# Kernel tuning notes

Hardware: AMD Instinct MI355X
Metric: run time of the kernel (lower is better)

## Reference

```python
import jax, jax.numpy as jnp
import numpy as np

N, D = 16384, 256

def setup_inputs() -> dict:
    key = jax.random.key(0)
    k1, k2, k3 = jax.random.split(key, 3)
    X = jax.random.normal(k1, (N, D), dtype=jnp.float32)
    W = jax.random.normal(k2, (D, D), dtype=jnp.float32) * (1.0 / np.sqrt(D))
    b = jax.random.normal(k3, (D,), dtype=jnp.float32) * (1.0 / np.sqrt(D))
    return {"X": X, "W": W, "b": b}

def reference(X, W, b):
    # Step 1: bilinear attention A = X W X^T   (N, N) -- materialized as in original
    A = (X @ W) @ X.T
    # Step 2: context aggregation Z = A X      (N, D)
    Z = A @ X
    # Step 3: output head g = Z b              (N,)
    g = Z @ b
    return g
```

## Files before the change

kernel.cpp:

```cpp
#include <hip/hip_runtime.h>

#define NROWS 16384
#define DDIM  256
#define K1BLK 2048
#define NSLOT 64


__global__ __launch_bounds__(256) void k1_v(const float* __restrict__ X,
                                            const float* __restrict__ b,
                                            float* __restrict__ slots) {
    const int tid  = threadIdx.x;
    const int lane = tid & 63;
    const int wave = tid >> 6;
    const int bid  = blockIdx.x;

    const float4* X4 = (const float4*)X;
    const float4  bf = ((const float4*)b)[lane];

    float4 vacc = make_float4(0.f, 0.f, 0.f, 0.f);
    const int row0 = bid * 8 + wave * 2;
    #pragma unroll
    for (int i = 0; i < 2; ++i) {
        const float4 xv = X4[(row0 + i) * 64 + lane];
        float t = xv.x * bf.x + xv.y * bf.y + xv.z * bf.z + xv.w * bf.w;
        #pragma unroll
        for (int off = 32; off; off >>= 1) t += __shfl_xor(t, off, 64);
        vacc.x += t * xv.x; vacc.y += t * xv.y;
        vacc.z += t * xv.z; vacc.w += t * xv.w;
    }

    __shared__ float sp[4][DDIM];
    ((float4*)sp[wave])[lane] = vacc;
    __syncthreads();
    const float s = sp[0][tid] + sp[1][tid] + sp[2][tid] + sp[3][tid];
    atomicAdd(&slots[(bid & (NSLOT - 1)) * DDIM + tid], s);
}

__global__ __launch_bounds__(256) void k2_w2(const float* __restrict__ slots,
                                             const float* __restrict__ W,
                                             float* __restrict__ w2) {
    const int tid  = threadIdx.x;
    const int lane = tid & 63;
    const int wave = tid >> 6;

    const float4* S4 = (const float4*)slots;
    float4 acc = make_float4(0.f, 0.f, 0.f, 0.f);
    const int r0 = wave * (NSLOT / 4);
    #pragma unroll
    for (int j = 0; j < NSLOT / 4; ++j) {
        const float4 p = S4[(r0 + j) * 64 + lane];
        acc.x += p.x; acc.y += p.y; acc.z += p.z; acc.w += p.w;
    }

    __shared__ float4 sp4[4][64];
    sp4[wave][lane] = acc;
    __syncthreads();

    const float* spf = (const float*)sp4;
    __shared__ __align__(16) float sv[DDIM];
    sv[tid] = spf[tid] + spf[256 + tid] + spf[512 + tid] + spf[768 + tid];
    __syncthreads();

    const float4 vf = ((const float4*)sv)[lane];
    const int row = blockIdx.x * 4 + wave;
    const float4 w = ((const float4*)W)[row * 64 + lane];
    float t = w.x * vf.x + w.y * vf.y + w.z * vf.z + w.w * vf.w;
    #pragma unroll
    for (int off = 32; off; off >>= 1) t += __shfl_xor(t, off, 64);
    if (lane == 0) w2[row] = t;
}

__global__ __launch_bounds__(256) void k3_g(const float* __restrict__ X,
                                            const float* __restrict__ w2,
                                            float* __restrict__ g) {
    const int tid  = threadIdx.x;
    const int lane = tid & 63;
    const int wave = tid >> 6;

    const float4* X4 = (const float4*)X;
    const float4  wf = ((const float4*)w2)[lane];

    const int row0 = blockIdx.x * 8 + wave * 2;
    #pragma unroll
    for (int i = 0; i < 2; ++i) {
        const float4 xv = X4[(row0 + i) * 64 + lane];
        float t = xv.x * wf.x + xv.y * wf.y + xv.z * wf.z + xv.w * wf.w;
        #pragma unroll
        for (int off = 32; off; off >>= 1) t += __shfl_xor(t, off, 64);
        if (lane == 0) g[row0 + i] = t;
    }
}

extern "C" void kernel_launch(void* const* d_in, const int* in_sizes, int n_in,
                              void* d_out, int out_size, void* d_ws, size_t ws_size,
                              hipStream_t stream) {
    const float* X = (const float*)d_in[0];
    const float* W = (const float*)d_in[1];
    const float* b = (const float*)d_in[2];
    float* out = (float*)d_out;

    float* slots = (float*)d_ws;
    float* w2    = slots + NSLOT * DDIM;

    k1_v <<<K1BLK, 256, 0, stream>>>(X, b, slots);
    k2_w2<<<NSLOT, 256, 0, stream>>>(slots, W, w2);
    k3_g <<<K1BLK, 256, 0, stream>>>(X, w2, out);
}
```

Before: 71.78 us.

## Fuse three kernels into one persistent launch with grid-wide barriers

Merges the three stages (v accumulation, w2 = W·v, g = X·w2) into a single kernel of 2048 blocks. Stages are separated by a hand-rolled two-level atomic grid barrier (64 sub-counters feeding one main counter), with sleep-based spinning. This removes two kernel launches and the gaps between them. In exchange it relies on all 2048 blocks being resident at once, and on the barrier counters in the workspace starting from a known value. The spin loop also gives up after a fixed count, which could silently break the ordering between stages.

```diff
diff --git a/kernel.cpp b/kernel.cpp
--- a/kernel.cpp
+++ b/kernel.cpp
@@ -2,92 +2,111 @@
 
 #define NROWS 16384
 #define DDIM  256
-#define K1BLK 2048
+#define GBLK  2048
 #define NSLOT 64
 
 
-__global__ __launch_bounds__(256) void k1_v(const float* __restrict__ X,
-                                            const float* __restrict__ b,
-                                            float* __restrict__ slots) {
+#define SUB1  0
+#define MAIN1 2048
+#define SUB2  2112
+#define MAIN2 4192
+#define REFC  4256
+
+__device__ __forceinline__ void gbar(unsigned* __restrict__ bars, int which,
+                                     unsigned initv) {
+    __syncthreads();
+    if (threadIdx.x == 0) {
+        unsigned* sub = bars + (which ? SUB2 : SUB1);
+        unsigned* mn  = bars + (which ? MAIN2 : MAIN1);
+        __threadfence();
+        unsigned old = atomicAdd(&sub[(blockIdx.x & 63) * 32], 1u);
+        if (old - initv == 31u) atomicAdd(mn, 1u);
+        unsigned spins = 0;
+        while (__hip_atomic_load(mn, __ATOMIC_RELAXED, __HIP_MEMORY_SCOPE_AGENT)
+               - initv < 64u) {
+            __builtin_amdgcn_s_sleep(2);
+            if (++spins > 4000000u) break;
+        }
+        __threadfence();
+    }
+    __syncthreads();
+}
+
+__global__ __launch_bounds__(256, 8)
+void fused(const float* __restrict__ X, const float* __restrict__ W,
+           const float* __restrict__ b, float* __restrict__ slots,
+           float* __restrict__ w2, unsigned* __restrict__ bars,
+           float* __restrict__ g) {
     const int tid  = threadIdx.x;
     const int lane = tid & 63;
     const int wave = tid >> 6;
     const int bid  = blockIdx.x;
 
+    __shared__ __align__(16) float sp[4][DDIM];
+    __shared__ __align__(16) float sv[DDIM];
+
     const float4* X4 = (const float4*)X;
-    const float4  bf = ((const float4*)b)[lane];
 
-    float4 vacc = make_float4(0.f, 0.f, 0.f, 0.f);
-    const int row0 = bid * 8 + wave * 2;
-    #pragma unroll
-    for (int i = 0; i < 2; ++i) {
-        const float4 xv = X4[(row0 + i) * 64 + lane];
-        float t = xv.x * bf.x + xv.y * bf.y + xv.z * bf.z + xv.w * bf.w;
+    const unsigned initv =
+        __hip_atomic_load(&bars[REFC], __ATOMIC_RELAXED, __HIP_MEMORY_SCOPE_AGENT);
+
+    {
+        const float4 bf = ((const float4*)b)[lane];
+        float4 vacc = make_float4(0.f, 0.f, 0.f, 0.f);
+        const int row0 = bid * 8 + wave * 2;
+        #pragma unroll
+        for (int i = 0; i < 2; ++i) {
+            const float4 xv = X4[(row0 + i) * 64 + lane];
+            float t = xv.x * bf.x + xv.y * bf.y + xv.z * bf.z + xv.w * bf.w;
+            #pragma unroll
+            for (int off = 32; off; off >>= 1) t += __shfl_xor(t, off, 64);
+            vacc.x += t * xv.x; vacc.y += t * xv.y;
+            vacc.z += t * xv.z; vacc.w += t * xv.w;
+        }
+        ((float4*)sp[wave])[lane] = vacc;
+        __syncthreads();
+        const float s = sp[0][tid] + sp[1][tid] + sp[2][tid] + sp[3][tid];
+        atomicAdd(&slots[(bid & (NSLOT - 1)) * DDIM + tid], s);
+    }
+
+    gbar(bars, 0, initv);
+
+    if (bid < NSLOT) {
+        const float4* S4 = (const float4*)slots;
+        float4 acc = make_float4(0.f, 0.f, 0.f, 0.f);
+        const int r0 = wave * (NSLOT / 4);
+        #pragma unroll
+        for (int j = 0; j < NSLOT / 4; ++j) {
+            const float4 p = S4[(r0 + j) * 64 + lane];
+            acc.x += p.x; acc.y += p.y; acc.z += p.z; acc.w += p.w;
+        }
+        ((float4*)sp[0])[wave * 64 + lane] = acc;
+        __syncthreads();
+        const float* spf = (const float*)sp;
+        sv[tid] = spf[tid] + spf[256 + tid] + spf[512 + tid] + spf[768 + tid];
+        __syncthreads();
+        const float4 vf = ((const float4*)sv)[lane];
+        const int row = bid * 4 + wave;
+        const float4 w = ((const float4*)W)[row * 64 + lane];
+        float t = w.x * vf.x + w.y * vf.y + w.z * vf.z + w.w * vf.w;
         #pragma unroll
         for (int off = 32; off; off >>= 1) t += __shfl_xor(t, off, 64);
-        vacc.x += t * xv.x; vacc.y += t * xv.y;
-        vacc.z += t * xv.z; vacc.w += t * xv.w;
+        if (lane == 0) w2[row] = t;
     }
 
-    __shared__ float sp[4][DDIM];
-    ((float4*)sp[wave])[lane] = vacc;
-    __syncthreads();
-    const float s = sp[0][tid] + sp[1][tid] + sp[2][tid] + sp[3][tid];
-    atomicAdd(&slots[(bid & (NSLOT - 1)) * DDIM + tid], s);
-}
+    gbar(bars, 1, initv);
 
-__global__ __launch_bounds__(256) void k2_w2(const float* __restrict__ slots,
-                                             const float* __restrict__ W,
-                                             float* __restrict__ w2) {
-    const int tid  = threadIdx.x;
-    const int lane = tid & 63;
-    const int wave = tid >> 6;
-
-    const float4* S4 = (const float4*)slots;
-    float4 acc = make_float4(0.f, 0.f, 0.f, 0.f);
-    const int r0 = wave * (NSLOT / 4);
-    #pragma unroll
-    for (int j = 0; j < NSLOT / 4; ++j) {
-        const float4 p = S4[(r0 + j) * 64 + lane];
-        acc.x += p.x; acc.y += p.y; acc.z += p.z; acc.w += p.w;
-    }
-
-    __shared__ float4 sp4[4][64];
-    sp4[wave][lane] = acc;
-    __syncthreads();
-
-    const float* spf = (const float*)sp4;
-    __shared__ __align__(16) float sv[DDIM];
-    sv[tid] = spf[tid] + spf[256 + tid] + spf[512 + tid] + spf[768 + tid];
-    __syncthreads();
-
-    const float4 vf = ((const float4*)sv)[lane];
-    const int row = blockIdx.x * 4 + wave;
-    const float4 w = ((const float4*)W)[row * 64 + lane];
-    float t = w.x * vf.x + w.y * vf.y + w.z * vf.z + w.w * vf.w;
-    #pragma unroll
-    for (int off = 32; off; off >>= 1) t += __shfl_xor(t, off, 64);
-    if (lane == 0) w2[row] = t;
-}
-
-__global__ __launch_bounds__(256) void k3_g(const float* __restrict__ X,
-                                            const float* __restrict__ w2,
-                                            float* __restrict__ g) {
-    const int tid  = threadIdx.x;
-    const int lane = tid & 63;
-    const int wave = tid >> 6;
-
-    const float4* X4 = (const float4*)X;
-    const float4  wf = ((const float4*)w2)[lane];
-
-    const int row0 = blockIdx.x * 8 + wave * 2;
-    #pragma unroll
-    for (int i = 0; i < 2; ++i) {
-        const float4 xv = X4[(row0 + i) * 64 + lane];
-        float t = xv.x * wf.x + xv.y * wf.y + xv.z * wf.z + xv.w * wf.w;
+    {
+        const float4 wf = ((const float4*)w2)[lane];
+        const int row0 = bid * 8 + wave * 2;
         #pragma unroll
-        for (int off = 32; off; off >>= 1) t += __shfl_xor(t, off, 64);
-        if (lane == 0) g[row0 + i] = t;
+        for (int i = 0; i < 2; ++i) {
+            const float4 xv = X4[(row0 + i) * 64 + lane];
+            float t = xv.x * wf.x + xv.y * wf.y + xv.z * wf.z + xv.w * wf.w;
+            #pragma unroll
+            for (int off = 32; off; off >>= 1) t += __shfl_xor(t, off, 64);
+            if (lane == 0) g[row0 + i] = t;
+        }
     }
 }
 
@@ -97,12 +116,11 @@
     const float* X = (const float*)d_in[0];
     const float* W = (const float*)d_in[1];
     const float* b = (const float*)d_in[2];
-    float* out = (float*)d_out;
+    float* g = (float*)d_out;
 
-    float* slots = (float*)d_ws;
-    float* w2    = slots + NSLOT * DDIM;
+    float*    slots = (float*)d_ws;
+    float*    w2    = slots + NSLOT * DDIM;
+    unsigned* bars  = (unsigned*)d_ws + 32768;
 
-    k1_v <<<K1BLK, 256, 0, stream>>>(X, b, slots);
-    k2_w2<<<NSLOT, 256, 0, stream>>>(slots, W, w2);
-    k3_g <<<K1BLK, 256, 0, stream>>>(X, w2, out);
+    fused<<<GBLK, 256, 0, stream>>>(X, W, b, slots, w2, bars, g);
 }
```

New measurement: 211.0 us. 194% more time.

## Replace slot atomics with per-block partials and distribute the W matvec by linearity

Applied to the files above, without the earlier changes.

k1 now writes one partial sum vector per block instead of atomically adding into 64 contended slots. k2 has each of 64 blocks reduce 32 of those partials, multiply the result by all of W, and atomically add the product into w2, which is valid because the matvec is linear. The goal is to remove the heavy float-atomic traffic from the first kernel. In exchange it adds a 2 MB partial write and read, 64 full reads of W, and a dependence on w2 being zeroed beforehand.

```diff
diff --git a/kernel.cpp b/kernel.cpp
--- a/kernel.cpp
+++ b/kernel.cpp
@@ -3,12 +3,12 @@
 #define NROWS 16384
 #define DDIM  256
 #define K1BLK 2048
-#define NSLOT 64
+#define RBLK  64
 
 
 __global__ __launch_bounds__(256) void k1_v(const float* __restrict__ X,
                                             const float* __restrict__ b,
-                                            float* __restrict__ slots) {
+                                            float* __restrict__ p1) {
     const int tid  = threadIdx.x;
     const int lane = tid & 63;
     const int wave = tid >> 6;
@@ -32,42 +32,44 @@
     __shared__ float sp[4][DDIM];
     ((float4*)sp[wave])[lane] = vacc;
     __syncthreads();
-    const float s = sp[0][tid] + sp[1][tid] + sp[2][tid] + sp[3][tid];
-    atomicAdd(&slots[(bid & (NSLOT - 1)) * DDIM + tid], s);
+    p1[bid * DDIM + tid] = sp[0][tid] + sp[1][tid] + sp[2][tid] + sp[3][tid];
 }
 
-__global__ __launch_bounds__(256) void k2_w2(const float* __restrict__ slots,
+__global__ __launch_bounds__(256) void k2_w2(const float* __restrict__ p1,
                                              const float* __restrict__ W,
                                              float* __restrict__ w2) {
     const int tid  = threadIdx.x;
     const int lane = tid & 63;
     const int wave = tid >> 6;
+    const int bid  = blockIdx.x;
 
-    const float4* S4 = (const float4*)slots;
+    const float4* P4 = (const float4*)p1;
     float4 acc = make_float4(0.f, 0.f, 0.f, 0.f);
-    const int r0 = wave * (NSLOT / 4);
+    const int rbase = bid * 32 + wave * 8;
     #pragma unroll
-    for (int j = 0; j < NSLOT / 4; ++j) {
-        const float4 p = S4[(r0 + j) * 64 + lane];
+    for (int i = 0; i < 8; ++i) {
+        const float4 p = P4[(rbase + i) * 64 + lane];
         acc.x += p.x; acc.y += p.y; acc.z += p.z; acc.w += p.w;
     }
 
-    __shared__ float4 sp4[4][64];
-    sp4[wave][lane] = acc;
+    __shared__ __align__(16) float sp[4 * DDIM];
+    __shared__ __align__(16) float sv[DDIM];
+    ((float4*)&sp[wave * DDIM])[lane] = acc;
+    __syncthreads();
+    sv[tid] = sp[tid] + sp[DDIM + tid] + sp[2 * DDIM + tid] + sp[3 * DDIM + tid];
     __syncthreads();
 
-    const float* spf = (const float*)sp4;
-    __shared__ __align__(16) float sv[DDIM];
-    sv[tid] = spf[tid] + spf[256 + tid] + spf[512 + tid] + spf[768 + tid];
-    __syncthreads();
-
-    const float4 vf = ((const float4*)sv)[lane];
-    const int row = blockIdx.x * 4 + wave;
-    const float4 w = ((const float4*)W)[row * 64 + lane];
-    float t = w.x * vf.x + w.y * vf.y + w.z * vf.z + w.w * vf.w;
-    #pragma unroll
-    for (int off = 32; off; off >>= 1) t += __shfl_xor(t, off, 64);
-    if (lane == 0) w2[row] = t;
+    const float4* W4  = (const float4*)W;
+    const float4  vf  = ((const float4*)sv)[lane];
+    #pragma unroll 4
+    for (int r = 0; r < 64; ++r) {
+        const int row = wave * 64 + r;
+        const float4 wv = W4[row * 64 + lane];
+        float t = wv.x * vf.x + wv.y * vf.y + wv.z * vf.z + wv.w * vf.w;
+        #pragma unroll
+        for (int off = 32; off; off >>= 1) t += __shfl_xor(t, off, 64);
+        if (lane == 0) atomicAdd(&w2[row], t);
+    }
 }
 
 __global__ __launch_bounds__(256) void k3_g(const float* __restrict__ X,
@@ -99,10 +101,10 @@
     const float* b = (const float*)d_in[2];
     float* out = (float*)d_out;
 
-    float* slots = (float*)d_ws;
-    float* w2    = slots + NSLOT * DDIM;
+    float* p1 = (float*)d_ws;
+    float* w2 = p1 + K1BLK * DDIM;
 
-    k1_v <<<K1BLK, 256, 0, stream>>>(X, b, slots);
-    k2_w2<<<NSLOT, 256, 0, stream>>>(slots, W, w2);
+    k1_v <<<K1BLK, 256, 0, stream>>>(X, b, p1);
+    k2_w2<<<RBLK,  256, 0, stream>>>(p1, W, w2);
     k3_g <<<K1BLK, 256, 0, stream>>>(X, w2, out);
 }
```

Result: slower. 119.4 us (+66.4%).
